# Optimization experiments

Hardware: AMD Instinct MI355X
Metric: run time of the kernel (lower is better)

## Reference

```python
import jax, jax.numpy as jnp
import numpy as np

BINS = 10

def setup_inputs() -> dict:
    key = jax.random.key(0)
    k1, k2 = jax.random.split(key)
    N, C = 262144, 80
    pred = jax.random.normal(k1, (N, C), dtype=jnp.float32)
    target = jax.random.randint(k2, (N, C), 0, 2, dtype=jnp.int32)
    return {"pred": pred, "target": target}


def _ghmc_loss(pred, target):
    # NOTE: faithful to the original torch code, which applies sigmoid to pred
    # and then feeds that *through binary_cross_entropy_with_logits* (i.e. the
    # sigmoid output is treated as logits -- a double sigmoid quirk we preserve).
    z = jax.nn.sigmoid(pred)                      # [N, C] "logits" fed to BCE-with-logits
    t = target.astype(z.dtype)                    # [N, C]
    # gradient magnitude, detached like pred.detach() in torch
    g = jnp.abs(jax.lax.stop_gradient(z) - t)     # in [0, 1]
    # label_weight is overwritten with ones in the original forward, so every
    # element is valid: tot = N * C.
    tot = jnp.asarray(z.size, dtype=z.dtype)

    # uniform bins: edges[i] = i/BINS, last edge nudged by 1e-6 so g == 1 lands
    # in the last bin -> equivalent to floor(g*BINS) clipped to BINS-1.
    idx = jnp.clip((g * BINS).astype(jnp.int32), 0, BINS - 1)   # [N, C]
    counts = jax.ops.segment_sum(
        jnp.ones((z.size,), dtype=z.dtype), idx.reshape(-1), num_segments=BINS
    )                                                            # [BINS]
    n_nonempty = jnp.sum(counts > 0).astype(z.dtype)
    per_bin_w = jnp.where(counts > 0, tot / jnp.maximum(counts, 1.0), 0.0)  # [BINS]
    weights = per_bin_w[idx] / jnp.maximum(n_nonempty, 1.0)      # [N, C]
    weights = jax.lax.stop_gradient(weights)

    # BCE-with-logits(z, t) = softplus(z) - t*z (numerically stable)
    bce = jax.nn.softplus(z) - t * z
    return jnp.sum(weights * bce) / tot


def reference(pred, target):
    return _ghmc_loss(pred, target)
```

## Files before the change

kernel.cpp:

```cpp
#include <hip/hip_runtime.h>


#define NBINS  10
#define GRID1  2048
#define BLOCK1 256

typedef float vf4 __attribute__((ext_vector_type(4)));
typedef int   vi4 __attribute__((ext_vector_type(4)));

#if __has_builtin(__builtin_amdgcn_exp2f)
__device__ __forceinline__ float nexp2(float a) { return __builtin_amdgcn_exp2f(a); }
#else
__device__ __forceinline__ float nexp2(float a) { return __expf(a * 0.69314718055994531f); }
#endif
#if __has_builtin(__builtin_amdgcn_logf)
__device__ __forceinline__ float nlog2(float a) { return __builtin_amdgcn_logf(a); }
#else
__device__ __forceinline__ float nlog2(float a) { return __logf(a) * 1.44269504088896341f; }
#endif

#define LOG2E 1.44269504088896341f
#define LN2   0.69314718055994531f

__global__ __launch_bounds__(BLOCK1) void ghmc_pass1(
    const vf4* __restrict__ pred4,
    const vi4* __restrict__ targ4,
    float* __restrict__ partial_s,
    int*   __restrict__ partial_c,
    int nvec4)
{
    __shared__ float sred[BLOCK1 / 64][NBINS];
    __shared__ int   cred[BLOCK1 / 64][NBINS];

    float s[NBINS];
#pragma unroll
    for (int b = 0; b < NBINS; ++b) s[b] = 0.0f;
    unsigned long long cnt = 0;

    const int idx    = blockIdx.x * BLOCK1 + threadIdx.x;
    const int stride = GRID1 * BLOCK1;

    int i = idx;
    for (; i + stride < nvec4; i += 2 * stride) {
        vf4 p0 = pred4[i];
        vi4 t0 = targ4[i];
        vf4 p1 = pred4[i + stride];
        vi4 t1 = targ4[i + stride];
        asm volatile("" : "+v"(p0), "+v"(t0), "+v"(p1), "+v"(t1));

        float x[8], tf[8];
#pragma unroll
        for (int j = 0; j < 4; ++j) {
            x[j]      = p0[j];  tf[j]     = (float)t0[j];
            x[4 + j]  = p1[j];  tf[4 + j] = (float)t1[j];
        }

        float z[8];
#pragma unroll
        for (int j = 0; j < 8; ++j)
            z[j] = __builtin_amdgcn_rcpf(1.0f + nexp2(-x[j] * LOG2E));
        asm volatile("" : "+v"(z[0]), "+v"(z[1]), "+v"(z[2]), "+v"(z[3]),
                         "+v"(z[4]), "+v"(z[5]), "+v"(z[6]), "+v"(z[7]));

        int bi[8]; float bce[8];
#pragma unroll
        for (int j = 0; j < 8; ++j) {
            float g = fabsf(z[j] - tf[j]);
            int   b = (int)(g * 10.0f);
            bi[j]   = b > (NBINS - 1) ? (NBINS - 1) : b;
            float sp = nlog2(1.0f + nexp2(z[j] * LOG2E)) * LN2;
            bce[j]  = sp - tf[j] * z[j];
        }
        asm volatile("" : "+v"(bce[0]), "+v"(bce[1]), "+v"(bce[2]), "+v"(bce[3]),
                         "+v"(bce[4]), "+v"(bce[5]), "+v"(bce[6]), "+v"(bce[7]),
                         "+v"(bi[0]), "+v"(bi[1]), "+v"(bi[2]), "+v"(bi[3]),
                         "+v"(bi[4]), "+v"(bi[5]), "+v"(bi[6]), "+v"(bi[7]));

#pragma unroll
        for (int j = 0; j < 8; ++j) {
#pragma unroll
            for (int b = 0; b < NBINS; ++b)
                s[b] += (bi[j] == b) ? bce[j] : 0.0f;
            cnt += 1ull << (6 * bi[j]);
        }
    }
    if (i < nvec4) {
        vf4 p0 = pred4[i];
        vi4 t0 = targ4[i];
#pragma unroll
        for (int j = 0; j < 4; ++j) {
            float tfj = (float)t0[j];
            float zj  = __builtin_amdgcn_rcpf(1.0f + nexp2(-p0[j] * LOG2E));
            float g   = fabsf(zj - tfj);
            int   b   = (int)(g * 10.0f);
            b = b > (NBINS - 1) ? (NBINS - 1) : b;
            float bc  = nlog2(1.0f + nexp2(zj * LOG2E)) * LN2 - tfj * zj;
#pragma unroll
            for (int bb = 0; bb < NBINS; ++bb)
                s[bb] += (b == bb) ? bc : 0.0f;
            cnt += 1ull << (6 * b);
        }
    }

    int c[NBINS];
#pragma unroll
    for (int b = 0; b < NBINS; ++b) c[b] = (int)((cnt >> (6 * b)) & 63ull);

#pragma unroll
    for (int b = 0; b < NBINS; ++b) {
#pragma unroll
        for (int off = 32; off > 0; off >>= 1) {
            s[b] += __shfl_down(s[b], off, 64);
            c[b] += __shfl_down(c[b], off, 64);
        }
    }

    const int wave = threadIdx.x >> 6;
    if ((threadIdx.x & 63) == 0) {
#pragma unroll
        for (int b = 0; b < NBINS; ++b) { sred[wave][b] = s[b]; cred[wave][b] = c[b]; }
    }
    __syncthreads();
    if (threadIdx.x < NBINS) {
        int b = threadIdx.x;
        partial_s[b * GRID1 + blockIdx.x] = sred[0][b] + sred[1][b] + sred[2][b] + sred[3][b];
        partial_c[b * GRID1 + blockIdx.x] = cred[0][b] + cred[1][b] + cred[2][b] + cred[3][b];
    }
}

#define BLOCK2 1024

__global__ __launch_bounds__(BLOCK2) void ghmc_pass2(
    const float* __restrict__ partial_s,
    const int*   __restrict__ partial_c,
    float* __restrict__ out,
    int nblocks)
{
    double as[NBINS];
    int    ac[NBINS];
#pragma unroll
    for (int b = 0; b < NBINS; ++b) { as[b] = 0.0; ac[b] = 0; }

    for (int j = threadIdx.x; j < nblocks; j += BLOCK2) {
#pragma unroll
        for (int b = 0; b < NBINS; ++b) {
            as[b] += (double)partial_s[b * nblocks + j];
            ac[b] += partial_c[b * nblocks + j];
        }
    }

#pragma unroll
    for (int b = 0; b < NBINS; ++b) {
#pragma unroll
        for (int off = 32; off > 0; off >>= 1) {
            as[b] += __shfl_down(as[b], off, 64);
            ac[b] += __shfl_down(ac[b], off, 64);
        }
    }

    __shared__ double sds[BLOCK2 / 64][NBINS];
    __shared__ int    sdc[BLOCK2 / 64][NBINS];
    int wave = threadIdx.x >> 6;
    if ((threadIdx.x & 63) == 0) {
#pragma unroll
        for (int b = 0; b < NBINS; ++b) { sds[wave][b] = as[b]; sdc[wave][b] = ac[b]; }
    }
    __syncthreads();

    if (threadIdx.x == 0) {
        int nn = 0;
        double acc = 0.0;
#pragma unroll
        for (int b = 0; b < NBINS; ++b) {
            double sb = 0.0;
            int    cb = 0;
#pragma unroll
            for (int w = 0; w < BLOCK2 / 64; ++w) { sb += sds[w][b]; cb += sdc[w][b]; }
            if (cb > 0) { nn += 1; acc += sb / (double)cb; }
        }
        out[0] = (float)(acc / (double)(nn > 0 ? nn : 1));
    }
}

extern "C" void kernel_launch(void* const* d_in, const int* in_sizes, int n_in,
                              void* d_out, int out_size, void* d_ws, size_t ws_size,
                              hipStream_t stream)
{
    const float* pred = (const float*)d_in[0];
    const int*   targ = (const int*)d_in[1];
    float*       out  = (float*)d_out;

    const int n     = in_sizes[0];
    const int nvec4 = n / 4;

    float* partial_s = (float*)d_ws;
    int*   partial_c = (int*)((char*)d_ws + GRID1 * NBINS * sizeof(float));

    ghmc_pass1<<<GRID1, BLOCK1, 0, stream>>>(
        (const vf4*)pred, (const vi4*)targ, partial_s, partial_c, nvec4);

    ghmc_pass2<<<1, BLOCK2, 0, stream>>>(partial_s, partial_c, out, GRID1);
}
```

Before: 197.2 us.

## Double-buffer pass1 input loads through LDS with async global_load_lds

Replaces direct vector register loads of pred and target with asynchronous global-to-LDS copies (global_load_lds, 16 bytes per lane) into a two-slot LDS ring. The next tile's load overlaps with the current tile's math. The per-iteration work drops from 8 to 4 elements per thread, and a block barrier is added every tile. The goal is to hide global memory latency, at the cost of extra LDS traffic, more barriers and less per-thread ILP in what may be a compute-heavy loop.

```diff
diff --git a/kernel.cpp b/kernel.cpp
--- a/kernel.cpp
+++ b/kernel.cpp
@@ -22,6 +22,11 @@
 #define LOG2E 1.44269504088896341f
 #define LN2   0.69314718055994531f
 
+#define GLOAD16(gsrc, ldst)                                                \
+    __builtin_amdgcn_global_load_lds(                                      \
+        (const __attribute__((address_space(1))) void*)(gsrc),             \
+        (__attribute__((address_space(3))) void*)(ldst), 16, 0, 0)
+
 __global__ __launch_bounds__(BLOCK1) void ghmc_pass1(
     const vf4* __restrict__ pred4,
     const vi4* __restrict__ targ4,
@@ -29,6 +34,8 @@
     int*   __restrict__ partial_c,
     int nvec4)
 {
+    __shared__ vf4  plds[2][BLOCK1];
+    __shared__ vi4  tlds[2][BLOCK1];
     __shared__ float sred[BLOCK1 / 64][NBINS];
     __shared__ int   cred[BLOCK1 / 64][NBINS];
 
@@ -37,69 +44,59 @@
     for (int b = 0; b < NBINS; ++b) s[b] = 0.0f;
     unsigned long long cnt = 0;
 
-    const int idx    = blockIdx.x * BLOCK1 + threadIdx.x;
+    const int tid    = threadIdx.x;
+    const int wbase  = tid & ~63;
+    const int g0     = blockIdx.x * BLOCK1 + tid;
     const int stride = GRID1 * BLOCK1;
-
-    int i = idx;
-    for (; i + stride < nvec4; i += 2 * stride) {
-        vf4 p0 = pred4[i];
-        vi4 t0 = targ4[i];
-        vf4 p1 = pred4[i + stride];
-        vi4 t1 = targ4[i + stride];
-        asm volatile("" : "+v"(p0), "+v"(t0), "+v"(p1), "+v"(t1));
-
-        float x[8], tf[8];
+    const int ntiles = nvec4 / stride;
+
+    auto group4 = [&](vf4 p, vi4 t) {
+        float z[4], tf[4];
 #pragma unroll
         for (int j = 0; j < 4; ++j) {
-            x[j]      = p0[j];  tf[j]     = (float)t0[j];
-            x[4 + j]  = p1[j];  tf[4 + j] = (float)t1[j];
-        }
-
-        float z[8];
-#pragma unroll
-        for (int j = 0; j < 8; ++j)
-            z[j] = __builtin_amdgcn_rcpf(1.0f + nexp2(-x[j] * LOG2E));
-        asm volatile("" : "+v"(z[0]), "+v"(z[1]), "+v"(z[2]), "+v"(z[3]),
-                         "+v"(z[4]), "+v"(z[5]), "+v"(z[6]), "+v"(z[7]));
-
-        int bi[8]; float bce[8];
-#pragma unroll
-        for (int j = 0; j < 8; ++j) {
+            tf[j] = (float)t[j];
+            z[j]  = __builtin_amdgcn_rcpf(1.0f + nexp2(-p[j] * LOG2E));
+        }
+        asm volatile("" : "+v"(z[0]), "+v"(z[1]), "+v"(z[2]), "+v"(z[3]));
+        int bi[4]; float bce[4];
+#pragma unroll
+        for (int j = 0; j < 4; ++j) {
             float g = fabsf(z[j] - tf[j]);
             int   b = (int)(g * 10.0f);
             bi[j]   = b > (NBINS - 1) ? (NBINS - 1) : b;
             float sp = nlog2(1.0f + nexp2(z[j] * LOG2E)) * LN2;
             bce[j]  = sp - tf[j] * z[j];
         }
-        asm volatile("" : "+v"(bce[0]), "+v"(bce[1]), "+v"(bce[2]), "+v"(bce[3]),
-                         "+v"(bce[4]), "+v"(bce[5]), "+v"(bce[6]), "+v"(bce[7]),
-                         "+v"(bi[0]), "+v"(bi[1]), "+v"(bi[2]), "+v"(bi[3]),
-                         "+v"(bi[4]), "+v"(bi[5]), "+v"(bi[6]), "+v"(bi[7]));
-
-#pragma unroll
-        for (int j = 0; j < 8; ++j) {
+#pragma unroll
+        for (int j = 0; j < 4; ++j) {
 #pragma unroll
             for (int b = 0; b < NBINS; ++b)
                 s[b] += (bi[j] == b) ? bce[j] : 0.0f;
             cnt += 1ull << (6 * bi[j]);
         }
-    }
-    if (i < nvec4) {
+    };
+
+    if (ntiles > 0) {
+        GLOAD16(&pred4[g0], &plds[0][wbase]);
+        GLOAD16(&targ4[g0], &tlds[0][wbase]);
+        __syncthreads();
+
+        int cur = 0;
+        for (int t = 0; t < ntiles; ++t) {
+            if (t + 1 < ntiles) {
+                const int gn = g0 + (t + 1) * stride;
+                GLOAD16(&pred4[gn], &plds[cur ^ 1][wbase]);
+                GLOAD16(&targ4[gn], &tlds[cur ^ 1][wbase]);
+            }
+            group4(plds[cur][tid], tlds[cur][tid]);
+            __syncthreads();
+            cur ^= 1;
+        }
+    }
+    for (int i = g0 + ntiles * stride; i < nvec4; i += stride) {
         vf4 p0 = pred4[i];
         vi4 t0 = targ4[i];
-#pragma unroll
-        for (int j = 0; j < 4; ++j) {
-            float tfj = (float)t0[j];
-            float zj  = __builtin_amdgcn_rcpf(1.0f + nexp2(-p0[j] * LOG2E));
-            float g   = fabsf(zj - tfj);
-            int   b   = (int)(g * 10.0f);
-            b = b > (NBINS - 1) ? (NBINS - 1) : b;
-            float bc  = nlog2(1.0f + nexp2(zj * LOG2E)) * LN2 - tfj * zj;
-#pragma unroll
-            for (int bb = 0; bb < NBINS; ++bb)
-                s[bb] += (b == bb) ? bc : 0.0f;
-            cnt += 1ull << (6 * b);
-        }
+        group4(p0, t0);
     }
 
     int c[NBINS];
@@ -115,14 +112,14 @@
         }
     }
 
-    const int wave = threadIdx.x >> 6;
-    if ((threadIdx.x & 63) == 0) {
+    const int wave = tid >> 6;
+    if ((tid & 63) == 0) {
 #pragma unroll
         for (int b = 0; b < NBINS; ++b) { sred[wave][b] = s[b]; cred[wave][b] = c[b]; }
     }
     __syncthreads();
-    if (threadIdx.x < NBINS) {
-        int b = threadIdx.x;
+    if (tid < NBINS) {
+        int b = tid;
         partial_s[b * GRID1 + blockIdx.x] = sred[0][b] + sred[1][b] + sred[2][b] + sred[3][b];
         partial_c[b * GRID1 + blockIdx.x] = cred[0][b] + cred[1][b] + cred[2][b] + cred[3][b];
     }
```

New measurement: 199.8 us. About the same (+1.3%).
